# Kernel tuning notes

Hardware: AMD Instinct MI355X
Metric: run time of the kernel (lower is better)

The kernel has to match this reference:

```python
import jax, jax.numpy as jnp
import numpy as np

THRESH = 0.5
MARGIN = 0.1
SCALE_POS = 2.0
SCALE_NEG = 40.0
EPSILON = 1e-5


def setup_inputs() -> dict:
    key = jax.random.key(0)
    kx, kl = jax.random.split(key)
    B, D, N_CLASSES = 4096, 1024, 256
    x = jax.random.normal(kx, (B, D), dtype=jnp.float32)
    # L2-normalize embeddings (standard for multi-similarity loss; keeps sim in [-1, 1])
    x = x / jnp.linalg.norm(x, axis=1, keepdims=True)
    labels = jax.random.randint(kl, (B,), 0, N_CLASSES, dtype=jnp.int64)
    return {"x": x, "labels": labels}


def reference(x, labels):
    B = x.shape[0]
    sim = jnp.matmul(x, x.T)  # [B, B]

    eye = jnp.eye(B, dtype=bool)
    same = labels[:, None] == labels[None, :]
    pos_mask = same & ~eye                      # positives excl. self
    neg_mask = ~same                            # negatives
    pos_valid = pos_mask & (sim < 1.0 - EPSILON)  # pos_pair_ after < 1-eps filter

    # per-row hardest stats (inf/-inf where empty)
    min_pos = jnp.min(jnp.where(pos_valid, sim, jnp.inf), axis=1)   # min over pos_pair_
    max_neg = jnp.max(jnp.where(neg_mask, sim, -jnp.inf), axis=1)   # max over neg_pair_

    # mined pairs
    neg_keep = neg_mask & (sim + MARGIN > min_pos[:, None])
    pos_keep = pos_valid & (sim - MARGIN < max_neg[:, None])

    has_row = (pos_valid.any(axis=1) & neg_mask.any(axis=1)
               & pos_keep.any(axis=1) & neg_keep.any(axis=1))

    pos_sum = jnp.sum(jnp.where(pos_keep, jnp.exp(-SCALE_POS * (sim - THRESH)), 0.0), axis=1)
    neg_sum = jnp.sum(jnp.where(neg_keep, jnp.exp(SCALE_NEG * (sim - THRESH)), 0.0), axis=1)

    pos_loss = jnp.log1p(pos_sum) / SCALE_POS
    neg_loss = jnp.log1p(neg_sum) / SCALE_NEG

    row_loss = jnp.where(has_row, pos_loss + neg_loss, 0.0)
    return jnp.sum(row_loss) / B
```

## Files before the change

### kernel.cpp

```cpp
#include <hip/hip_runtime.h>
#include <hip/hip_bf16.h>
#include <math.h>
#include <stdint.h>


#define THRESH    0.5f
#define MARGIN    0.1f
#define SCALE_POS 2.0f
#define SCALE_NEG 40.0f
#define POS_CAP   (1.0f - 1e-5f)

typedef __bf16 bf16x8 __attribute__((ext_vector_type(8)));
typedef float  f32x4  __attribute__((ext_vector_type(4)));

__device__ __forceinline__ uint16_t f2bf(float f) {
  union { float f; uint32_t u; } v; v.f = f;
  uint32_t u = v.u;
  u += 0x7FFFu + ((u >> 16) & 1u);
  return (uint16_t)(u >> 16);
}

__global__ __launch_bounds__(256) void cvt_bf16_kernel(
    const float* __restrict__ x, uint16_t* __restrict__ y, int n) {
  int i = (blockIdx.x * 256 + threadIdx.x) * 4;
  if (i + 3 < n) {
    float4 v = *(const float4*)(x + i);
    ushort4 o;
    o.x = f2bf(v.x); o.y = f2bf(v.y); o.z = f2bf(v.z); o.w = f2bf(v.w);
    *(ushort4*)(y + i) = o;
  }
}

__device__ __forceinline__ unsigned fkey(float f) {
  unsigned u = __float_as_uint(f);
  return (u & 0x80000000u) ? ~u : (u | 0x80000000u);
}
__device__ __forceinline__ float funkey(unsigned k) {
  unsigned u = (k & 0x80000000u) ? (k & 0x7FFFFFFFu) : ~k;
  return __uint_as_float(u);
}

#if defined(__has_builtin)
#if __has_builtin(__builtin_amdgcn_global_load_lds)
#define HAVE_GLL 1
#endif
#endif

__device__ __forceinline__ void stage16(const uint16_t* g, uint16_t* lds_wave_base, int lane) {
#ifdef HAVE_GLL
  __builtin_amdgcn_global_load_lds(
      (const __attribute__((address_space(1))) void*)g,
      (__attribute__((address_space(3))) void*)lds_wave_base, 16, 0, 0);
#else
  *(uint4*)(lds_wave_base + lane * 8) = *(const uint4*)g;
#endif
}

__global__ __launch_bounds__(256) void simgemm_mine_kernel(
    const uint16_t* __restrict__ X, const int* __restrict__ labels,
    float* __restrict__ C, unsigned* __restrict__ minKey,
    unsigned* __restrict__ maxKey, int B, int D, int NT) {
  __shared__ __align__(16) uint16_t sA[128 * 32];
  __shared__ __align__(16) uint16_t sB[128 * 32];
  __shared__ int rowLab[128];
  __shared__ int colLab[128];

  int rem = blockIdx.x;
  int bi = 0;
  while (rem >= NT - bi) { rem -= NT - bi; ++bi; }
  const int bj = bi + rem;
  const bool diag = (bi == bj);

  const int tid  = threadIdx.x;
  const int wave = tid >> 6;
  const int lane = tid & 63;
  const int waveM = wave >> 1, waveN = wave & 1;
  const int bm = bi * 128;
  const int bn = bj * 128;

  if (tid < 128) rowLab[tid] = labels[bm + tid];
  else           colLab[tid - 128] = labels[bn + tid - 128];

  const int ch0 = tid;
  const int ch1 = tid + 256;
  const int r0 = ch0 >> 2, c0 = (ch0 & 3) * 8;
  const int r1 = ch1 >> 2, c1 = (ch1 & 3) * 8;

  const uint16_t* gA = X + (size_t)bm * D;
  const uint16_t* gB = X + (size_t)bn * D;

  uint16_t* lA0 = sA + wave * 512;
  uint16_t* lA1 = sA + 2048 + wave * 512;
  uint16_t* lB0 = sB + wave * 512;
  uint16_t* lB1 = sB + 2048 + wave * 512;

  const int fr = lane & 15;
  const int fq = lane >> 4;
  const int aoff = (waveM * 64 + fr) * 32 + fq * 8;
  const int boff = (waveN * 64 + fr) * 32 + fq * 8;

  const uint16_t* sBsrc = diag ? sA : sB;

  f32x4 acc[4][4] = {};

  for (int k0 = 0; k0 < D; k0 += 32) {
    stage16(gA + (size_t)r0 * D + k0 + c0, lA0, lane);
    stage16(gA + (size_t)r1 * D + k0 + c1, lA1, lane);
    if (!diag) {
      stage16(gB + (size_t)r0 * D + k0 + c0, lB0, lane);
      stage16(gB + (size_t)r1 * D + k0 + c1, lB1, lane);
    }
    __syncthreads();

    bf16x8 af[4], bfv[4];
#pragma unroll
    for (int t = 0; t < 4; ++t) af[t]  = *(const bf16x8*)(sA + aoff + t * 512);
#pragma unroll
    for (int t = 0; t < 4; ++t) bfv[t] = *(const bf16x8*)(sBsrc + boff + t * 512);

#pragma unroll
    for (int mt = 0; mt < 4; ++mt)
#pragma unroll
      for (int nt = 0; nt < 4; ++nt)
        acc[mt][nt] = __builtin_amdgcn_mfma_f32_16x16x32_bf16(
            af[mt], bfv[nt], acc[mt][nt], 0, 0, 0);
    __syncthreads();
  }

#pragma unroll
  for (int mt = 0; mt < 4; ++mt)
#pragma unroll
    for (int nt = 0; nt < 4; ++nt) {
      const int col = bn + waveN * 64 + nt * 16 + fr;
#pragma unroll
      for (int r = 0; r < 4; ++r) {
        const int row = bm + waveM * 64 + mt * 16 + fq * 4 + r;
        C[(size_t)row * B + col] = acc[mt][nt][r];
      }
    }

  int labC[4]; float cMin[4], cMax[4];
#pragma unroll
  for (int nt = 0; nt < 4; ++nt) {
    labC[nt] = colLab[waveN * 64 + nt * 16 + fr];
    cMin[nt] = 1e30f; cMax[nt] = -1e30f;
  }

#pragma unroll
  for (int mt = 0; mt < 4; ++mt) {
    float rMin[4], rMax[4]; int labR[4];
#pragma unroll
    for (int r = 0; r < 4; ++r) {
      labR[r] = rowLab[waveM * 64 + mt * 16 + fq * 4 + r];
      rMin[r] = 1e30f; rMax[r] = -1e30f;
    }
#pragma unroll
    for (int nt = 0; nt < 4; ++nt) {
      const int cl = waveN * 64 + nt * 16 + fr;
#pragma unroll
      for (int r = 0; r < 4; ++r) {
        const int rl = waveM * 64 + mt * 16 + fq * 4 + r;
        const float s = acc[mt][nt][r];
        if (labR[r] == labC[nt]) {
          if (!(diag && rl == cl) && s < POS_CAP) {
            rMin[r] = fminf(rMin[r], s);
            cMin[nt] = fminf(cMin[nt], s);
          }
        } else {
          rMax[r] = fmaxf(rMax[r], s);
          cMax[nt] = fmaxf(cMax[nt], s);
        }
      }
    }
#pragma unroll
    for (int m = 1; m < 16; m <<= 1)
#pragma unroll
      for (int r = 0; r < 4; ++r) {
        rMin[r] = fminf(rMin[r], __shfl_xor(rMin[r], m, 64));
        rMax[r] = fmaxf(rMax[r], __shfl_xor(rMax[r], m, 64));
      }
    if (fr == 0) {
#pragma unroll
      for (int r = 0; r < 4; ++r) {
        const int row = bm + waveM * 64 + mt * 16 + fq * 4 + r;
        if (rMin[r] < 2.f)  atomicMin(&minKey[row], fkey(rMin[r]));
        if (rMax[r] > -2.f) atomicMax(&maxKey[row], fkey(rMax[r]));
      }
    }
  }

  if (!diag) {
#pragma unroll
    for (int m = 16; m < 64; m <<= 1)
#pragma unroll
      for (int nt = 0; nt < 4; ++nt) {
        cMin[nt] = fminf(cMin[nt], __shfl_xor(cMin[nt], m, 64));
        cMax[nt] = fmaxf(cMax[nt], __shfl_xor(cMax[nt], m, 64));
      }
    if (lane < 16) {
#pragma unroll
      for (int nt = 0; nt < 4; ++nt) {
        const int col = bn + waveN * 64 + nt * 16 + fr;
        if (cMin[nt] < 2.f)  atomicMin(&minKey[col], fkey(cMin[nt]));
        if (cMax[nt] > -2.f) atomicMax(&maxKey[col], fkey(cMax[nt]));
      }
    }
  }
}

__global__ __launch_bounds__(256) void exploss_kernel(
    const float* __restrict__ C, const int* __restrict__ labels,
    const unsigned* __restrict__ minKey, const unsigned* __restrict__ maxKey,
    float* __restrict__ psum, float* __restrict__ nsum, int B, int NT) {
  __shared__ int   rLab[32];
  __shared__ float rMinp[32], rMaxn[32];
  __shared__ int   cLab[128];
  __shared__ float cMinp[128], cMaxn[128];
  __shared__ float pCarr[128], nCarr[128];

  int rem = blockIdx.x >> 2;
  const int split = blockIdx.x & 3;
  int bi = 0;
  while (rem >= NT - bi) { rem -= NT - bi; ++bi; }
  const int bj = bi + rem;
  const bool diag = (bi == bj);
  const int bm = bi * 128, bn = bj * 128;
  const int rbase = split * 32;

  const int tid = threadIdx.x;
  if (tid < 32) {
    const int row = bm + rbase + tid;
    rLab[tid]  = labels[row];
    rMinp[tid] = funkey(minKey[row]);
    rMaxn[tid] = funkey(maxKey[row]);
  } else if (tid < 160) {
    const int col = bn + (tid - 32);
    cLab[tid - 32]  = labels[col];
    cMinp[tid - 32] = funkey(minKey[col]);
    cMaxn[tid - 32] = funkey(maxKey[col]);
  }
  if (tid < 128) { pCarr[tid] = 0.f; nCarr[tid] = 0.f; }
  __syncthreads();

  const int rowg = tid >> 5;
  const int c0   = (tid & 31) * 4;
  int labC[4]; float mpC[4], mnC[4];
#pragma unroll
  for (int q = 0; q < 4; ++q) {
    labC[q] = cLab[c0 + q]; mpC[q] = cMinp[c0 + q]; mnC[q] = cMaxn[c0 + q];
  }
  float pCa[4] = {0.f, 0.f, 0.f, 0.f}, nCa[4] = {0.f, 0.f, 0.f, 0.f};

  for (int it = 0; it < 4; ++it) {
    const int rr = rowg + it * 8;
    const int rl = rbase + rr;
    const float4 v = *(const float4*)(C + (size_t)(bm + rl) * B + bn + c0);
    const float sq[4] = {v.x, v.y, v.z, v.w};
    const int   lr  = rLab[rr];
    const float rmn = rMaxn[rr];
    const float rmp = rMinp[rr];
    float pR = 0.f, nR = 0.f;
#pragma unroll
    for (int q = 0; q < 4; ++q) {
      const float s = sq[q];
      if (lr == labC[q]) {
        if (!(diag && rl == c0 + q) && s < POS_CAP) {
          const float e = __expf(-SCALE_POS * (s - THRESH));
          if (s - MARGIN < rmn)    pR += e;
          if (s - MARGIN < mnC[q]) pCa[q] += e;
        }
      } else {
        const float e = __expf(SCALE_NEG * (s - THRESH));
        if (s + MARGIN > rmp)    nR += e;
        if (s + MARGIN > mpC[q]) nCa[q] += e;
      }
    }
#pragma unroll
    for (int m = 1; m < 32; m <<= 1) {
      pR += __shfl_xor(pR, m, 64);
      nR += __shfl_xor(nR, m, 64);
    }
    if ((tid & 31) == 0) {
      atomicAdd(&psum[bm + rl], pR);
      atomicAdd(&nsum[bm + rl], nR);
    }
  }

  if (!diag) {
#pragma unroll
    for (int q = 0; q < 4; ++q) {
      atomicAdd(&pCarr[c0 + q], pCa[q]);
      atomicAdd(&nCarr[c0 + q], nCa[q]);
    }
    __syncthreads();
    if (tid < 128) {
      if (pCarr[tid] != 0.f) atomicAdd(&psum[bn + tid], pCarr[tid]);
      if (nCarr[tid] != 0.f) atomicAdd(&nsum[bn + tid], nCarr[tid]);
    }
  }
}

__global__ __launch_bounds__(1024) void final_kernel(
    const unsigned* __restrict__ minKey, const unsigned* __restrict__ maxKey,
    const float* __restrict__ psum, const float* __restrict__ nsum,
    float* __restrict__ out, int B) {
  __shared__ float red[16];
  const int tid = threadIdx.x;
  float acc = 0.f;
  for (int i = tid; i < B; i += 1024) {
    const unsigned mk = minKey[i], xk = maxKey[i];
    const float p = psum[i], n = nsum[i];
    if (mk != 0xFFFFFFFFu && xk != 0u && p > 0.f && n > 0.f)
      acc += log1pf(p) * (1.0f / SCALE_POS) + log1pf(n) * (1.0f / SCALE_NEG);
  }
#pragma unroll
  for (int m = 32; m > 0; m >>= 1) acc += __shfl_xor(acc, m, 64);
  if ((tid & 63) == 0) red[tid >> 6] = acc;
  __syncthreads();
  if (tid == 0) {
    float t = 0.f;
#pragma unroll
    for (int w = 0; w < 16; ++w) t += red[w];
    out[0] = t / (float)B;
  }
}

extern "C" void kernel_launch(void* const* d_in, const int* in_sizes, int n_in,
                              void* d_out, int out_size, void* d_ws, size_t ws_size,
                              hipStream_t stream) {
  const float* x      = (const float*)d_in[0];
  const int*   labels = (const int*)d_in[1];
  float*       out    = (float*)d_out;

  const int B = in_sizes[1];
  const int D = in_sizes[0] / B;
  const int NT = B / 128;
  const int NTILES = NT * (NT + 1) / 2;

  uint16_t* xbf = (uint16_t*)d_ws;
  size_t xbytes = (((size_t)B * D * 2) + 255) & ~(size_t)255;
  float* sim = (float*)((char*)d_ws + xbytes);
  size_t simbytes = (size_t)B * B * 4;
  unsigned* minKey = (unsigned*)((char*)d_ws + xbytes + simbytes);
  unsigned* maxKey = minKey + B;
  float* psumA = (float*)(maxKey + B);
  float* nsumA = psumA + B;

  hipMemsetAsync(minKey, 0xFF, (size_t)B * 4, stream);
  hipMemsetAsync(maxKey, 0x00, (size_t)B * 12, stream);

  const int n = B * D;
  cvt_bf16_kernel<<<n / 1024, 256, 0, stream>>>(x, xbf, n);

  simgemm_mine_kernel<<<NTILES, 256, 0, stream>>>(xbf, labels, sim, minKey, maxKey, B, D, NT);
  exploss_kernel<<<NTILES * 4, 256, 0, stream>>>(sim, labels, minKey, maxKey, psumA, nsumA, B, NT);
  final_kernel<<<1, 1024, 0, stream>>>(minKey, maxKey, psumA, nsumA, out, B);
}
```

Before: 152.4 us.

## Fuse sim GEMM, mining, and exp-loss into one cooperative kernel with grid sync

Adds a cooperative fused kernel that keeps each 128x128 similarity tile in registers, does the row/column hard mining with atomics, runs a grid-wide sync, then computes the exp-weighted positive and negative sums from the same registers. This removes the write and re-read of the full BxB float similarity matrix and one kernel launch. The cost is a grid barrier, which requires all 528 tiles to be co-resident; an occupancy check falls back to the old two-kernel path otherwise. The GEMM loop is single-buffered with two barriers per k-step.

```diff
diff --git a/kernel.cpp b/kernel.cpp
--- a/kernel.cpp
+++ b/kernel.cpp
@@ -1,7 +1,10 @@
 #include <hip/hip_runtime.h>
 #include <hip/hip_bf16.h>
+#include <hip/hip_cooperative_groups.h>
 #include <math.h>
 #include <stdint.h>
+
+namespace cg = cooperative_groups;
 
 
 #define THRESH    0.5f
@@ -56,6 +59,226 @@
 #endif
 }
 
+__global__ __launch_bounds__(256, 3) void fused_kernel(
+    const uint16_t* __restrict__ X, const int* __restrict__ labels,
+    unsigned* __restrict__ minKey, unsigned* __restrict__ maxKey,
+    float* __restrict__ psum, float* __restrict__ nsum,
+    int B, int D, int NT) {
+  __shared__ __align__(16) uint16_t sA[128 * 32];
+  __shared__ __align__(16) uint16_t sB[128 * 32];
+  __shared__ int rowLab[128], colLab[128];
+  __shared__ float rMinp[128], rMaxn[128], cMinp[128], cMaxn[128];
+
+  int rem = blockIdx.x;
+  int bi = 0;
+  while (rem >= NT - bi) { rem -= NT - bi; ++bi; }
+  const int bj = bi + rem;
+  const bool diag = (bi == bj);
+
+  const int tid  = threadIdx.x;
+  const int wave = tid >> 6;
+  const int lane = tid & 63;
+  const int waveM = wave >> 1, waveN = wave & 1;
+  const int bm = bi * 128;
+  const int bn = bj * 128;
+
+  if (tid < 128) rowLab[tid] = labels[bm + tid];
+  else           colLab[tid - 128] = labels[bn + tid - 128];
+
+  const int r0 = tid >> 2,         c0 = (tid & 3) * 8;
+  const int r1 = (tid + 256) >> 2, c1 = (tid & 3) * 8;
+
+  const uint16_t* gA = X + (size_t)bm * D;
+  const uint16_t* gB = X + (size_t)bn * D;
+
+  uint16_t* lA0 = sA + wave * 512;
+  uint16_t* lA1 = sA + 2048 + wave * 512;
+  uint16_t* lB0 = sB + wave * 512;
+  uint16_t* lB1 = sB + 2048 + wave * 512;
+
+  const int fr = lane & 15;
+  const int fq = lane >> 4;
+  const int aoff = (waveM * 64 + fr) * 32 + fq * 8;
+  const int boff = (waveN * 64 + fr) * 32 + fq * 8;
+
+  const uint16_t* sBsrc = diag ? sA : sB;
+
+  f32x4 acc[4][4] = {};
+
+  for (int k0 = 0; k0 < D; k0 += 32) {
+    stage16(gA + (size_t)r0 * D + k0 + c0, lA0, lane);
+    stage16(gA + (size_t)r1 * D + k0 + c1, lA1, lane);
+    if (!diag) {
+      stage16(gB + (size_t)r0 * D + k0 + c0, lB0, lane);
+      stage16(gB + (size_t)r1 * D + k0 + c1, lB1, lane);
+    }
+    __syncthreads();
+
+    bf16x8 af[4], bfv[4];
+#pragma unroll
+    for (int t = 0; t < 4; ++t) af[t]  = *(const bf16x8*)(sA + aoff + t * 512);
+#pragma unroll
+    for (int t = 0; t < 4; ++t) bfv[t] = *(const bf16x8*)(sBsrc + boff + t * 512);
+
+#pragma unroll
+    for (int mt = 0; mt < 4; ++mt)
+#pragma unroll
+      for (int nt = 0; nt < 4; ++nt)
+        acc[mt][nt] = __builtin_amdgcn_mfma_f32_16x16x32_bf16(
+            af[mt], bfv[nt], acc[mt][nt], 0, 0, 0);
+    __syncthreads();
+  }
+
+  int labC[4];
+#pragma unroll
+  for (int nt = 0; nt < 4; ++nt) labC[nt] = colLab[waveN * 64 + nt * 16 + fr];
+
+  {
+    float cMin[4], cMax[4];
+#pragma unroll
+    for (int nt = 0; nt < 4; ++nt) { cMin[nt] = 1e30f; cMax[nt] = -1e30f; }
+
+#pragma unroll
+    for (int mt = 0; mt < 4; ++mt) {
+      float rMin[4], rMax[4]; int labR[4];
+#pragma unroll
+      for (int r = 0; r < 4; ++r) {
+        labR[r] = rowLab[waveM * 64 + mt * 16 + fq * 4 + r];
+        rMin[r] = 1e30f; rMax[r] = -1e30f;
+      }
+#pragma unroll
+      for (int nt = 0; nt < 4; ++nt) {
+        const int cl = waveN * 64 + nt * 16 + fr;
+#pragma unroll
+        for (int r = 0; r < 4; ++r) {
+          const int rl = waveM * 64 + mt * 16 + fq * 4 + r;
+          const float s = acc[mt][nt][r];
+          if (labR[r] == labC[nt]) {
+            if (!(diag && rl == cl) && s < POS_CAP) {
+              rMin[r] = fminf(rMin[r], s);
+              cMin[nt] = fminf(cMin[nt], s);
+            }
+          } else {
+            rMax[r] = fmaxf(rMax[r], s);
+            cMax[nt] = fmaxf(cMax[nt], s);
+          }
+        }
+      }
+#pragma unroll
+      for (int m = 1; m < 16; m <<= 1)
+#pragma unroll
+        for (int r = 0; r < 4; ++r) {
+          rMin[r] = fminf(rMin[r], __shfl_xor(rMin[r], m, 64));
+          rMax[r] = fmaxf(rMax[r], __shfl_xor(rMax[r], m, 64));
+        }
+      if (fr == 0) {
+#pragma unroll
+        for (int r = 0; r < 4; ++r) {
+          const int row = bm + waveM * 64 + mt * 16 + fq * 4 + r;
+          if (rMin[r] < 2.f)  atomicMin(&minKey[row], fkey(rMin[r]));
+          if (rMax[r] > -2.f) atomicMax(&maxKey[row], fkey(rMax[r]));
+        }
+      }
+    }
+
+    if (!diag) {
+#pragma unroll
+      for (int m = 16; m < 64; m <<= 1)
+#pragma unroll
+        for (int nt = 0; nt < 4; ++nt) {
+          cMin[nt] = fminf(cMin[nt], __shfl_xor(cMin[nt], m, 64));
+          cMax[nt] = fmaxf(cMax[nt], __shfl_xor(cMax[nt], m, 64));
+        }
+      if (lane < 16) {
+#pragma unroll
+        for (int nt = 0; nt < 4; ++nt) {
+          const int col = bn + waveN * 64 + nt * 16 + fr;
+          if (cMin[nt] < 2.f)  atomicMin(&minKey[col], fkey(cMin[nt]));
+          if (cMax[nt] > -2.f) atomicMax(&maxKey[col], fkey(cMax[nt]));
+        }
+      }
+    }
+  }
+
+  cg::this_grid().sync();
+
+  if (tid < 128) {
+    rMinp[tid] = funkey(minKey[bm + tid]);
+    rMaxn[tid] = funkey(maxKey[bm + tid]);
+  } else {
+    cMinp[tid - 128] = funkey(minKey[bn + tid - 128]);
+    cMaxn[tid - 128] = funkey(maxKey[bn + tid - 128]);
+  }
+  __syncthreads();
+
+  float pCol[4] = {0.f, 0.f, 0.f, 0.f}, nCol[4] = {0.f, 0.f, 0.f, 0.f};
+
+#pragma unroll
+  for (int mt = 0; mt < 4; ++mt) {
+    float pRow[4] = {0.f, 0.f, 0.f, 0.f}, nRow[4] = {0.f, 0.f, 0.f, 0.f};
+    int labR[4]; float rmn[4], rmp[4];
+#pragma unroll
+    for (int r = 0; r < 4; ++r) {
+      const int rl = waveM * 64 + mt * 16 + fq * 4 + r;
+      labR[r] = rowLab[rl]; rmn[r] = rMaxn[rl]; rmp[r] = rMinp[rl];
+    }
+#pragma unroll
+    for (int nt = 0; nt < 4; ++nt) {
+      const int cl = waveN * 64 + nt * 16 + fr;
+      const float cmn = cMaxn[cl], cmp = cMinp[cl];
+#pragma unroll
+      for (int r = 0; r < 4; ++r) {
+        const int rl = waveM * 64 + mt * 16 + fq * 4 + r;
+        const float s = acc[mt][nt][r];
+        if (labR[r] == labC[nt]) {
+          if (!(diag && rl == cl) && s < POS_CAP) {
+            const float e = __expf(-SCALE_POS * (s - THRESH));
+            if (s - MARGIN < rmn[r]) pRow[r] += e;
+            if (s - MARGIN < cmn)    pCol[nt] += e;
+          }
+        } else {
+          const float e = __expf(SCALE_NEG * (s - THRESH));
+          if (s + MARGIN > rmp[r]) nRow[r] += e;
+          if (s + MARGIN > cmp)    nCol[nt] += e;
+        }
+      }
+    }
+#pragma unroll
+    for (int m = 1; m < 16; m <<= 1)
+#pragma unroll
+      for (int r = 0; r < 4; ++r) {
+        pRow[r] += __shfl_xor(pRow[r], m, 64);
+        nRow[r] += __shfl_xor(nRow[r], m, 64);
+      }
+    if (fr == 0) {
+#pragma unroll
+      for (int r = 0; r < 4; ++r) {
+        const int row = bm + waveM * 64 + mt * 16 + fq * 4 + r;
+        if (pRow[r] != 0.f) atomicAdd(&psum[row], pRow[r]);
+        if (nRow[r] != 0.f) atomicAdd(&nsum[row], nRow[r]);
+      }
+    }
+  }
+
+  if (!diag) {
+#pragma unroll
+    for (int m = 16; m < 64; m <<= 1)
+#pragma unroll
+      for (int nt = 0; nt < 4; ++nt) {
+        pCol[nt] += __shfl_xor(pCol[nt], m, 64);
+        nCol[nt] += __shfl_xor(nCol[nt], m, 64);
+      }
+    if (lane < 16) {
+#pragma unroll
+      for (int nt = 0; nt < 4; ++nt) {
+        const int col = bn + waveN * 64 + nt * 16 + fr;
+        if (pCol[nt] != 0.f) atomicAdd(&psum[col], pCol[nt]);
+        if (nCol[nt] != 0.f) atomicAdd(&nsum[col], nCol[nt]);
+      }
+    }
+  }
+}
+
 __global__ __launch_bounds__(256) void simgemm_mine_kernel(
     const uint16_t* __restrict__ X, const int* __restrict__ labels,
     float* __restrict__ C, unsigned* __restrict__ minKey,
@@ -81,10 +304,8 @@
   if (tid < 128) rowLab[tid] = labels[bm + tid];
   else           colLab[tid - 128] = labels[bn + tid - 128];
 
-  const int ch0 = tid;
-  const int ch1 = tid + 256;
-  const int r0 = ch0 >> 2, c0 = (ch0 & 3) * 8;
-  const int r1 = ch1 >> 2, c1 = (ch1 & 3) * 8;
+  const int r0 = tid >> 2,         c0 = (tid & 3) * 8;
+  const int r1 = (tid + 256) >> 2, c1 = (tid & 3) * 8;
 
   const uint16_t* gA = X + (size_t)bm * D;
   const uint16_t* gB = X + (size_t)bn * D;
@@ -332,19 +553,18 @@
   const int*   labels = (const int*)d_in[1];
   float*       out    = (float*)d_out;
 
-  const int B = in_sizes[1];
-  const int D = in_sizes[0] / B;
-  const int NT = B / 128;
+  int B = in_sizes[1];
+  int D = in_sizes[0] / B;
+  int NT = B / 128;
   const int NTILES = NT * (NT + 1) / 2;
 
   uint16_t* xbf = (uint16_t*)d_ws;
   size_t xbytes = (((size_t)B * D * 2) + 255) & ~(size_t)255;
-  float* sim = (float*)((char*)d_ws + xbytes);
-  size_t simbytes = (size_t)B * B * 4;
-  unsigned* minKey = (unsigned*)((char*)d_ws + xbytes + simbytes);
+  unsigned* minKey = (unsigned*)((char*)d_ws + xbytes);
   unsigned* maxKey = minKey + B;
   float* psumA = (float*)(maxKey + B);
   float* nsumA = psumA + B;
+  float* sim   = (float*)((char*)d_ws + xbytes + ((size_t)B * 16 + 255 & ~(size_t)255));
 
   hipMemsetAsync(minKey, 0xFF, (size_t)B * 4, stream);
   hipMemsetAsync(maxKey, 0x00, (size_t)B * 12, stream);
@@ -352,7 +572,21 @@
   const int n = B * D;
   cvt_bf16_kernel<<<n / 1024, 256, 0, stream>>>(x, xbf, n);
 
-  simgemm_mine_kernel<<<NTILES, 256, 0, stream>>>(xbf, labels, sim, minKey, maxKey, B, D, NT);
-  exploss_kernel<<<NTILES * 4, 256, 0, stream>>>(sim, labels, minKey, maxKey, psumA, nsumA, B, NT);
+  int perMP = 0;
+  hipOccupancyMaxActiveBlocksPerMultiprocessor(&perMP, fused_kernel, 256, 0);
+  int numMP = 0;
+  hipDeviceGetAttribute(&numMP, hipDeviceAttributeMultiprocessorCount, 0);
+  const bool coop_ok = (perMP > 0 && numMP > 0 && (long)perMP * numMP >= NTILES);
+
+  if (coop_ok) {
+    void* args[] = {(void*)&xbf, (void*)&labels, (void*)&minKey, (void*)&maxKey,
+                    (void*)&psumA, (void*)&nsumA, (void*)&B, (void*)&D, (void*)&NT};
+    hipLaunchCooperativeKernel((void*)fused_kernel, dim3(NTILES), dim3(256),
+                               args, 0, stream);
+  } else {
+    simgemm_mine_kernel<<<NTILES, 256, 0, stream>>>(xbf, labels, sim, minKey, maxKey, B, D, NT);
+    exploss_kernel<<<NTILES * 4, 256, 0, stream>>>(sim, labels, minKey, maxKey, psumA, nsumA, B, NT);
+  }
+
   final_kernel<<<1, 1024, 0, stream>>>(minKey, maxKey, psumA, nsumA, out, B);
 }
```

Result: no change. 151.2 us (-0.8%).
